# Performance work log

Measured on AMD Instinct MI355X. Metric: run time of the kernel, lower is better.

## Reference

```python
import jax, jax.numpy as jnp
import numpy as np

B, D_ENC, T = 4, 512, 200
D_DEC, U = 640, 100
H, V = 640, 1025


def setup_inputs() -> dict:
    key = jax.random.key(0)
    ks = jax.random.split(key, 8)
    s = lambda k, shape, fan: jax.random.normal(k, shape, dtype=jnp.float32) / np.sqrt(fan)
    return {
        "encoder_outputs": jax.random.normal(ks[0], (B, D_ENC, T), dtype=jnp.float32),
        "decoder_outputs": jax.random.normal(ks[1], (B, D_DEC, U), dtype=jnp.float32),
        "W_enc": s(ks[2], (D_ENC, H), D_ENC),
        "b_enc": jnp.zeros((H,), dtype=jnp.float32),
        "W_pred": s(ks[3], (D_DEC, H), D_DEC),
        "b_pred": jnp.zeros((H,), dtype=jnp.float32),
        "W_out": s(ks[4], (H, V), H),
        "b_out": jnp.zeros((V,), dtype=jnp.float32),
    }


def reference(encoder_outputs, decoder_outputs, W_enc, b_enc, W_pred, b_pred, W_out, b_out):
    # transpose(1,2): [B, D, T] -> [B, T, D], then linear projections to H
    enc_proj = jnp.einsum("bdt,dh->bth", encoder_outputs, W_enc) + b_enc   # [B, T, H]
    dec_proj = jnp.einsum("bdu,dh->buh", decoder_outputs, W_pred) + b_pred  # [B, U, H]
    # broadcast-sum: [B, T, 1, H] + [B, 1, U, H] -> [B, T, U, H]
    x = enc_proj[:, :, None, :] + dec_proj[:, None, :, :]
    x = jax.nn.relu(x)           # joint_net[0] activation; joint_net[1] dropout = identity (eval)
    out = jnp.einsum("btuh,hv->btuv", x, W_out) + b_out  # [B, T, U, V]
    return out
```

## Files before the change

kernel.cpp:

```cpp
#include <hip/hip_runtime.h>
#include <hip/hip_bf16.h>

#define B_   4
#define DENC 512
#define T_   200
#define DDEC 640
#define U_   100
#define H_   640
#define V_   1025
#define VPAD 1152

typedef float f32x4 __attribute__((ext_vector_type(4)));
typedef _Float16 f16x8 __attribute__((ext_vector_type(8)));
typedef unsigned short u16x8 __attribute__((ext_vector_type(8)));

__device__ __forceinline__ uint4 addrelu16(uint4 e, uint4 d) {
    f16x8 ev = __builtin_bit_cast(f16x8, e);
    f16x8 dv = __builtin_bit_cast(f16x8, d);
    f16x8 s = ev + dv;
    f16x8 z = {(_Float16)0.f, (_Float16)0.f, (_Float16)0.f, (_Float16)0.f,
               (_Float16)0.f, (_Float16)0.f, (_Float16)0.f, (_Float16)0.f};
    s = __builtin_elementwise_max(s, z);
    return __builtin_bit_cast(uint4, s);
}

__device__ __forceinline__ void gload_lds16(const void* g, void* l) {
    __builtin_amdgcn_global_load_lds(
        (const __attribute__((address_space(1))) unsigned int*)g,
        (__attribute__((address_space(3))) unsigned int*)l, 16, 0, 0);
}

__global__ __launch_bounds__(256) void prep_fused_kernel(
    const float* __restrict__ enc, const float* __restrict__ W_enc,
    const float* __restrict__ b_enc,
    const float* __restrict__ dec, const float* __restrict__ W_pred,
    const float* __restrict__ b_pred,
    const float* __restrict__ W_out,
    _Float16* __restrict__ encP, _Float16* __restrict__ decP,
    _Float16* __restrict__ Wt)
{
    __shared__ float tile[64][65];
    int bx = blockIdx.x;
    int tid = threadIdx.x;

    if (bx < 260) {
        int b = bx / 65, r5 = bx % 65, hc = r5 / 13, tg = r5 % 13;
        int h  = hc * 128 + (tid & 127);
        int t0 = tg * 16 + (tid >> 7) * 8;
        if (t0 >= T_) return;
        const float* ec = enc + (size_t)b * DENC * T_ + t0;
        const float* Wc = W_enc + h;
        float acc[8] = {0.f,0.f,0.f,0.f,0.f,0.f,0.f,0.f};
        #pragma unroll 8
        for (int d = 0; d < DENC; ++d) {
            float w = Wc[(size_t)d * H_];
            float4 e0 = *(const float4*)(ec + (size_t)d * T_);
            float4 e1 = *(const float4*)(ec + (size_t)d * T_ + 4);
            acc[0] += w * e0.x; acc[1] += w * e0.y; acc[2] += w * e0.z; acc[3] += w * e0.w;
            acc[4] += w * e1.x; acc[5] += w * e1.y; acc[6] += w * e1.z; acc[7] += w * e1.w;
        }
        float bb = b_enc[h];
        #pragma unroll
        for (int i = 0; i < 8; ++i)
            encP[((size_t)b * T_ + t0 + i) * H_ + h] = (_Float16)(acc[i] + bb);
    } else if (bx < 520) {
        int i5 = bx - 260;
        int b = i5 / 65, r5 = i5 % 65, hc = r5 / 13, ug = r5 % 13;
        int h  = hc * 128 + (tid & 127);
        int u0 = ug * 8 + (tid >> 7) * 4;
        if (u0 >= U_) return;
        const float* dc = dec + (size_t)b * DDEC * U_ + u0;
        const float* Wc = W_pred + h;
        float acc[4] = {0.f,0.f,0.f,0.f};
        #pragma unroll 8
        for (int d = 0; d < DDEC; ++d) {
            float w = Wc[(size_t)d * H_];
            float4 e0 = *(const float4*)(dc + (size_t)d * U_);
            acc[0] += w * e0.x; acc[1] += w * e0.y; acc[2] += w * e0.z; acc[3] += w * e0.w;
        }
        float bb = b_pred[h];
        #pragma unroll
        for (int i = 0; i < 4; ++i)
            decP[((size_t)b * U_ + u0 + i) * H_ + h] = (_Float16)(acc[i] + bb);
    } else {
        int j = bx - 520;
        int hc = j / 18, vc = j % 18;
        int h0 = hc * 64, v0 = vc * 64;
        #pragma unroll
        for (int it = 0; it < 16; ++it) {
            int hl = it * 4 + (tid >> 6);
            int vl = tid & 63;
            int v = v0 + vl;
            tile[hl][vl] = (v < V_) ? W_out[(size_t)(h0 + hl) * V_ + v] : 0.f;
        }
        __syncthreads();
        #pragma unroll
        for (int it = 0; it < 16; ++it) {
            int vl = it * 4 + (tid >> 6);
            int hl = tid & 63;
            Wt[(size_t)(v0 + vl) * H_ + h0 + hl] = (_Float16)tile[hl][vl];
        }
    }
}

#define ESTR 260
__global__ __launch_bounds__(256) void joint_kernel(
    const unsigned short* __restrict__ encP,
    const unsigned short* __restrict__ decP,
    const unsigned short* __restrict__ Wt,
    const float* __restrict__ b_out,
    float* __restrict__ out)
{
    __shared__ uint4 LA[2][64][4];
    __shared__ uint4 LB[2][256][4];
    int tid = threadIdx.x;

    if (blockIdx.x >= 5200) {
        int idx = (blockIdx.x - 5200) * 256 + tid;
        if (idx >= B_ * T_ * U_) return;
        int u = idx % U_;
        int t = (idx / U_) % T_;
        int b = idx / (U_ * T_);
        const uint4* e = (const uint4*)(encP + ((size_t)b * T_ + t) * H_);
        const uint4* d = (const uint4*)(decP + ((size_t)b * U_ + u) * H_);
        const uint4* wv = (const uint4*)(Wt + (size_t)1024 * H_);
        float acc1 = 0.f;
        for (int c = 0; c < H_ / 8; ++c) {
            f16x8 x = __builtin_bit_cast(f16x8, addrelu16(e[c], d[c]));
            f16x8 wq = __builtin_bit_cast(f16x8, wv[c]);
            #pragma unroll
            for (int m = 0; m < 8; ++m)
                acc1 += (float)x[m] * (float)wq[m];
        }
        out[((size_t)(b * T_ + t) * U_ + u) * V_ + 1024] = acc1 + b_out[1024];
        return;
    }

    int f   = blockIdx.x;
    int n   = (f & 7) * 650 + (f >> 3);
    int vi  = n / 1300;
    int rem = n - vi * 1300;
    int b   = rem / 325;
    int tu  = rem - b * 325;

    int tt = tu / 13, ut = tu % 13;
    int t0 = tt * 8, u0 = ut * 8, vb = vi * 256;
    int lane = tid & 63, w = tid >> 6;
    int lrow = lane & 15, kg = lane >> 4;

    int r  = tid >> 2, kc = tid & 3;
    int ta = t0 + (r >> 3);
    int ua = u0 + (r & 7); if (ua > U_ - 1) ua = U_ - 1;
    const unsigned short* eR = encP + ((size_t)b * T_ + ta) * H_ + kc * 8;
    const unsigned short* dR = decP + ((size_t)b * U_ + ua) * H_ + kc * 8;
    int fA = (r >> 1) & 3;

    int pcB = lane & 3;
    const unsigned short* gB[4];
    #pragma unroll
    for (int m = 0; m < 4; ++m) {
        int cl = w * 64 + m * 16 + (lane >> 2);
        gB[m] = Wt + (size_t)(vb + cl) * H_ + (pcB ^ ((cl >> 1) & 3)) * 8;
    }

    f32x4 acc[4][4];
    #pragma unroll
    for (int i = 0; i < 4; ++i)
        #pragma unroll
        for (int j = 0; j < 4; ++j)
            acc[i][j] = (f32x4){0.f, 0.f, 0.f, 0.f};

    {
        uint4 E = *(const uint4*)(eR);
        uint4 D = *(const uint4*)(dR);
        LA[0][r][kc ^ fA] = addrelu16(E, D);
        #pragma unroll
        for (int m = 0; m < 4; ++m)
            gload_lds16(gB[m], &LB[0][w * 64 + m * 16][0]);
    }
    __syncthreads();

    #pragma unroll 2
    for (int kt = 0; kt < 20; ++kt) {
        int cur = kt & 1;
        uint4 En, Dn;
        if (kt < 19) {
            En = *(const uint4*)(eR + (kt + 1) * 32);
            Dn = *(const uint4*)(dR + (kt + 1) * 32);
            #pragma unroll
            for (int m = 0; m < 4; ++m)
                gload_lds16(gB[m] + (kt + 1) * 32, &LB[cur ^ 1][w * 64 + m * 16][0]);
        }
        f16x8 a[4], bq[4];
        #pragma unroll
        for (int i = 0; i < 4; ++i) {
            int row = i * 16 + lrow;
            a[i] = __builtin_bit_cast(f16x8, LA[cur][row][kg ^ ((row >> 1) & 3)]);
        }
        #pragma unroll
        for (int j = 0; j < 4; ++j) {
            int col = w * 64 + j * 16 + lrow;
            bq[j] = __builtin_bit_cast(f16x8, LB[cur][col][kg ^ ((col >> 1) & 3)]);
        }
        #pragma unroll
        for (int i = 0; i < 4; ++i)
            #pragma unroll
            for (int j = 0; j < 4; ++j)
                acc[i][j] = __builtin_amdgcn_mfma_f32_16x16x32_f16(a[i], bq[j], acc[i][j], 0, 0, 0);
        if (kt < 19)
            LA[cur ^ 1][r][kc ^ fA] = addrelu16(En, Dn);
        __syncthreads();
    }

    float* etile = (float*)LB;
    #pragma unroll
    for (int i = 0; i < 4; ++i) {
        __syncthreads();
        #pragma unroll
        for (int j = 0; j < 4; ++j) {
            int col = w * 64 + j * 16 + lrow;
            float bo = b_out[vb + col];
            #pragma unroll
            for (int q = 0; q < 4; ++q)
                etile[(kg * 4 + q) * ESTR + col] = acc[i][j][q] + bo;
        }
        __syncthreads();
        #pragma unroll
        for (int rr = 0; rr < 4; ++rr) {
            int row16 = w * 4 + rr;
            int row = i * 16 + row16;
            int t = t0 + (row >> 3);
            int u = u0 + (row & 7);
            if (u < U_) {
                float* ob = &out[(((size_t)b * T_ + t) * U_ + u) * V_ + vb];
                const float* lb = &etile[row16 * ESTR];
                #pragma unroll
                for (int it = 0; it < 4; ++it)
                    ob[it * 64 + lane] = lb[it * 64 + lane];
            }
        }
    }
}

extern "C" void kernel_launch(void* const* d_in, const int* in_sizes, int n_in,
                              void* d_out, int out_size, void* d_ws, size_t ws_size,
                              hipStream_t stream) {
    const float* enc    = (const float*)d_in[0];
    const float* dec    = (const float*)d_in[1];
    const float* W_enc  = (const float*)d_in[2];
    const float* b_enc  = (const float*)d_in[3];
    const float* W_pred = (const float*)d_in[4];
    const float* b_pred = (const float*)d_in[5];
    const float* W_out  = (const float*)d_in[6];
    const float* b_out  = (const float*)d_in[7];
    float* out = (float*)d_out;

    char* ws = (char*)d_ws;
    _Float16* encP = (_Float16*)ws;
    _Float16* decP = (_Float16*)(ws + 1024000);
    _Float16* Wt   = (_Float16*)(ws + 1024000 + 512000);

    prep_fused_kernel<<<dim3(700), 256, 0, stream>>>(
        enc, W_enc, b_enc, dec, W_pred, b_pred, W_out, encP, decP, Wt);
    joint_kernel<<<dim3(5200 + (B_ * T_ * U_ + 255) / 256), 256, 0, stream>>>(
        (const unsigned short*)encP, (const unsigned short*)decP,
        (const unsigned short*)Wt, b_out, out);
}
```

Before: 271.8 us.

## Keep full-K W_out slice resident in LDS and stream A fragments from registers

The joint GEMM is restructured so each 512-thread block loads a 64-column slice of Wt across the whole H dimension into 80KB of dynamic LDS once, with an XOR swizzle. Each wave then builds its A fragments directly in registers from global enc/dec rows, applying the add+relu per k-step with two-deep register prefetch, so the per-iteration LDS A staging and the block barriers go away. The tile shape changes to 256 (t,u) rows by 64 V columns, which gives 5824 blocks. The trade-off is much higher LDS use per block, which may limit occupancy, narrower 64-float output stores, and repeated global reads of enc/dec rows across the V blocks.

```diff
diff --git a/kernel.cpp b/kernel.cpp
--- a/kernel.cpp
+++ b/kernel.cpp
@@ -8,11 +8,9 @@
 #define U_   100
 #define H_   640
 #define V_   1025
-#define VPAD 1152
 
 typedef float f32x4 __attribute__((ext_vector_type(4)));
 typedef _Float16 f16x8 __attribute__((ext_vector_type(8)));
-typedef unsigned short u16x8 __attribute__((ext_vector_type(8)));
 
 __device__ __forceinline__ uint4 addrelu16(uint4 e, uint4 d) {
     f16x8 ev = __builtin_bit_cast(f16x8, e);
@@ -103,20 +101,18 @@
     }
 }
 
-#define ESTR 260
-__global__ __launch_bounds__(256) void joint_kernel(
+__global__ __launch_bounds__(512, 4) void joint_kernel(
     const unsigned short* __restrict__ encP,
     const unsigned short* __restrict__ decP,
     const unsigned short* __restrict__ Wt,
     const float* __restrict__ b_out,
     float* __restrict__ out)
 {
-    __shared__ uint4 LA[2][64][4];
-    __shared__ uint4 LB[2][256][4];
+    extern __shared__ char LDSRAW[];
     int tid = threadIdx.x;
 
-    if (blockIdx.x >= 5200) {
-        int idx = (blockIdx.x - 5200) * 256 + tid;
+    if (blockIdx.x >= 5824) {
+        int idx = (blockIdx.x - 5824) * 512 + tid;
         if (idx >= B_ * T_ * U_) return;
         int u = idx % U_;
         int t = (idx / U_) % T_;
@@ -136,109 +132,99 @@
         return;
     }
 
-    int f   = blockIdx.x;
-    int n   = (f & 7) * 650 + (f >> 3);
-    int vi  = n / 1300;
-    int rem = n - vi * 1300;
-    int b   = rem / 325;
-    int tu  = rem - b * 325;
-
-    int tt = tu / 13, ut = tu % 13;
-    int t0 = tt * 8, u0 = ut * 8, vb = vi * 256;
+    int f    = blockIdx.x;
+    int n    = (f & 7) * 728 + (f >> 3);
+    int vblk = n / 364;
+    int rem  = n - vblk * 364;
+    int b    = rem / 91;
+    int y    = rem - b * 91;
+    int tt = y / 13, ut = y % 13;
+    int t0 = tt * 32, u0 = ut * 8;
+    int vb = vblk * 64;
     int lane = tid & 63, w = tid >> 6;
     int lrow = lane & 15, kg = lane >> 4;
 
-    int r  = tid >> 2, kc = tid & 3;
-    int ta = t0 + (r >> 3);
-    int ua = u0 + (r & 7); if (ua > U_ - 1) ua = U_ - 1;
-    const unsigned short* eR = encP + ((size_t)b * T_ + ta) * H_ + kc * 8;
-    const unsigned short* dR = decP + ((size_t)b * U_ + ua) * H_ + kc * 8;
-    int fA = (r >> 1) & 3;
-
-    int pcB = lane & 3;
-    const unsigned short* gB[4];
+    {
+        char* ldsb = LDSRAW + w * 10240;
+        #pragma unroll
+        for (int m = 0; m < 10; ++m) {
+            int flat = m * 64 + lane;
+            int cl = flat / 80, p = flat % 80;
+            int c  = p ^ (cl & 7);
+            const unsigned short* src = Wt + (size_t)(vb + w * 8 + cl) * H_ + c * 8;
+            gload_lds16(src, ldsb + m * 1024);
+        }
+    }
+    __syncthreads();
+
+    int row0 = w * 32 + lrow;
+    int tA0 = t0 + (row0 >> 3);        if (tA0 > T_ - 1) tA0 = T_ - 1;
+    int tA1 = t0 + ((row0 + 16) >> 3); if (tA1 > T_ - 1) tA1 = T_ - 1;
+    int uA  = u0 + (lrow & 7);         if (uA  > U_ - 1) uA  = U_ - 1;
+    const uint4* e0p = (const uint4*)(encP + ((size_t)b * T_ + tA0) * H_) + kg;
+    const uint4* e1p = (const uint4*)(encP + ((size_t)b * T_ + tA1) * H_) + kg;
+    const uint4* dp  = (const uint4*)(decP + ((size_t)b * U_ + uA ) * H_) + kg;
+
+    const char* LBb = LDSRAW;
+    int sB = (lrow & 7) << 4;
+    int bbase[4];
     #pragma unroll
-    for (int m = 0; m < 4; ++m) {
-        int cl = w * 64 + m * 16 + (lane >> 2);
-        gB[m] = Wt + (size_t)(vb + cl) * H_ + (pcB ^ ((cl >> 1) & 3)) * 8;
-    }
-
-    f32x4 acc[4][4];
+    for (int j = 0; j < 4; ++j) bbase[j] = (j * 16 + lrow) * 1280;
+
+    f32x4 acc[2][4];
     #pragma unroll
-    for (int i = 0; i < 4; ++i)
+    for (int i = 0; i < 2; ++i)
         #pragma unroll
         for (int j = 0; j < 4; ++j)
             acc[i][j] = (f32x4){0.f, 0.f, 0.f, 0.f};
 
-    {
-        uint4 E = *(const uint4*)(eR);
-        uint4 D = *(const uint4*)(dR);
-        LA[0][r][kc ^ fA] = addrelu16(E, D);
-        #pragma unroll
-        for (int m = 0; m < 4; ++m)
-            gload_lds16(gB[m], &LB[0][w * 64 + m * 16][0]);
-    }
+    uint4 E0a = e0p[0], E1a = e1p[0], Da = dp[0];
+    uint4 E0b = e0p[4], E1b = e1p[4], Db = dp[4];
+
+    #pragma unroll 2
+    for (int ks = 0; ks < 20; ++ks) {
+        f16x8 a0 = __builtin_bit_cast(f16x8, addrelu16(E0a, Da));
+        f16x8 a1 = __builtin_bit_cast(f16x8, addrelu16(E1a, Da));
+        E0a = E0b; E1a = E1b; Da = Db;
+        if (ks < 18) {
+            E0b = e0p[(ks + 2) * 4];
+            E1b = e1p[(ks + 2) * 4];
+            Db  = dp[(ks + 2) * 4];
+        }
+        int xoff = ((ks * 4 + kg) << 4) ^ sB;
+        f16x8 bq[4];
+        #pragma unroll
+        for (int j = 0; j < 4; ++j)
+            bq[j] = *(const f16x8*)(LBb + bbase[j] + xoff);
+        #pragma unroll
+        for (int j = 0; j < 4; ++j) {
+            acc[0][j] = __builtin_amdgcn_mfma_f32_16x16x32_f16(a0, bq[j], acc[0][j], 0, 0, 0);
+            acc[1][j] = __builtin_amdgcn_mfma_f32_16x16x32_f16(a1, bq[j], acc[1][j], 0, 0, 0);
+        }
+    }
+
     __syncthreads();
-
-    #pragma unroll 2
-    for (int kt = 0; kt < 20; ++kt) {
-        int cur = kt & 1;
-        uint4 En, Dn;
-        if (kt < 19) {
-            En = *(const uint4*)(eR + (kt + 1) * 32);
-            Dn = *(const uint4*)(dR + (kt + 1) * 32);
-            #pragma unroll
-            for (int m = 0; m < 4; ++m)
-                gload_lds16(gB[m] + (kt + 1) * 32, &LB[cur ^ 1][w * 64 + m * 16][0]);
-        }
-        f16x8 a[4], bq[4];
-        #pragma unroll
-        for (int i = 0; i < 4; ++i) {
-            int row = i * 16 + lrow;
-            a[i] = __builtin_bit_cast(f16x8, LA[cur][row][kg ^ ((row >> 1) & 3)]);
-        }
+    float* etile = (float*)LDSRAW + (size_t)w * 1088;
+    #pragma unroll
+    for (int i = 0; i < 2; ++i) {
         #pragma unroll
         for (int j = 0; j < 4; ++j) {
-            int col = w * 64 + j * 16 + lrow;
-            bq[j] = __builtin_bit_cast(f16x8, LB[cur][col][kg ^ ((col >> 1) & 3)]);
-        }
-        #pragma unroll
-        for (int i = 0; i < 4; ++i)
-            #pragma unroll
-            for (int j = 0; j < 4; ++j)
-                acc[i][j] = __builtin_amdgcn_mfma_f32_16x16x32_f16(a[i], bq[j], acc[i][j], 0, 0, 0);
-        if (kt < 19)
-            LA[cur ^ 1][r][kc ^ fA] = addrelu16(En, Dn);
-        __syncthreads();
-    }
-
-    float* etile = (float*)LB;
-    #pragma unroll
-    for (int i = 0; i < 4; ++i) {
-        __syncthreads();
-        #pragma unroll
-        for (int j = 0; j < 4; ++j) {
-            int col = w * 64 + j * 16 + lrow;
+            int col = j * 16 + lrow;
             float bo = b_out[vb + col];
             #pragma unroll
             for (int q = 0; q < 4; ++q)
-                etile[(kg * 4 + q) * ESTR + col] = acc[i][j][q] + bo;
+                etile[(kg * 4 + q) * 68 + col] = acc[i][j][q] + bo;
         }
         __syncthreads();
         #pragma unroll
-        for (int rr = 0; rr < 4; ++rr) {
-            int row16 = w * 4 + rr;
-            int row = i * 16 + row16;
+        for (int rr = 0; rr < 16; ++rr) {
+            int row = w * 32 + i * 16 + rr;
             int t = t0 + (row >> 3);
             int u = u0 + (row & 7);
-            if (u < U_) {
-                float* ob = &out[(((size_t)b * T_ + t) * U_ + u) * V_ + vb];
-                const float* lb = &etile[row16 * ESTR];
-                #pragma unroll
-                for (int it = 0; it < 4; ++it)
-                    ob[it * 64 + lane] = lb[it * 64 + lane];
-            }
-        }
+            if (t < T_ && u < U_)
+                out[(((size_t)b * T_ + t) * U_ + u) * V_ + vb + lane] = etile[rr * 68 + lane];
+        }
+        __syncthreads();
     }
 }
 
@@ -260,9 +246,12 @@
     _Float16* decP = (_Float16*)(ws + 1024000);
     _Float16* Wt   = (_Float16*)(ws + 1024000 + 512000);
 
+    (void)hipFuncSetAttribute((const void*)joint_kernel,
+                              hipFuncAttributeMaxDynamicSharedMemorySize, 81920);
+
     prep_fused_kernel<<<dim3(700), 256, 0, stream>>>(
         enc, W_enc, b_enc, dec, W_pred, b_pred, W_out, encP, decP, Wt);
-    joint_kernel<<<dim3(5200 + (B_ * T_ * U_ + 255) / 256), 256, 0, stream>>>(
+    joint_kernel<<<dim3(5824 + 157), 512, 81920, stream>>>(
         (const unsigned short*)encP, (const unsigned short*)decP,
         (const unsigned short*)Wt, b_out, out);
 }
```

After: 333.8 us. +22.8%, slower.

## Split projection reduction across warps with LDS reduce in prep kernel

Applied to the files above, without the earlier changes.

The encoder and decoder projection blocks now split the D reduction across the four wavefronts, with each thread accumulating more time/unit columns. Partial sums go into shared memory and are combined before the fp16 store. This raises the number of prep blocks and gives more memory-level parallelism in the small-GEMM prologue. The cost is an extra LDS round trip and a barrier.

```diff
diff --git a/kernel.cpp b/kernel.cpp
--- a/kernel.cpp
+++ b/kernel.cpp
@@ -12,7 +12,6 @@
 
 typedef float f32x4 __attribute__((ext_vector_type(4)));
 typedef _Float16 f16x8 __attribute__((ext_vector_type(8)));
-typedef unsigned short u16x8 __attribute__((ext_vector_type(8)));
 
 __device__ __forceinline__ uint4 addrelu16(uint4 e, uint4 d) {
     f16x8 ev = __builtin_bit_cast(f16x8, e);
@@ -39,53 +38,115 @@
     _Float16* __restrict__ encP, _Float16* __restrict__ decP,
     _Float16* __restrict__ Wt)
 {
-    __shared__ float tile[64][65];
+    __shared__ float sbuf[4224];
     int bx = blockIdx.x;
     int tid = threadIdx.x;
-
-    if (bx < 260) {
-        int b = bx / 65, r5 = bx % 65, hc = r5 / 13, tg = r5 % 13;
-        int h  = hc * 128 + (tid & 127);
-        int t0 = tg * 16 + (tid >> 7) * 8;
-        if (t0 >= T_) return;
+    int lane = tid & 63, w = tid >> 6;
+
+    if (bx < 520) {
+        int b = bx / 130, r5 = bx % 130, hc = r5 / 13, tg = r5 % 13;
+        int h  = hc * 64 + lane;
+        int t0 = tg * 16;
+        const float* Wc = W_enc + h;
         const float* ec = enc + (size_t)b * DENC * T_ + t0;
-        const float* Wc = W_enc + h;
-        float acc[8] = {0.f,0.f,0.f,0.f,0.f,0.f,0.f,0.f};
-        #pragma unroll 8
-        for (int d = 0; d < DENC; ++d) {
-            float w = Wc[(size_t)d * H_];
-            float4 e0 = *(const float4*)(ec + (size_t)d * T_);
-            float4 e1 = *(const float4*)(ec + (size_t)d * T_ + 4);
-            acc[0] += w * e0.x; acc[1] += w * e0.y; acc[2] += w * e0.z; acc[3] += w * e0.w;
-            acc[4] += w * e1.x; acc[5] += w * e1.y; acc[6] += w * e1.z; acc[7] += w * e1.w;
-        }
-        float bb = b_enc[h];
-        #pragma unroll
-        for (int i = 0; i < 8; ++i)
-            encP[((size_t)b * T_ + t0 + i) * H_ + h] = (_Float16)(acc[i] + bb);
-    } else if (bx < 520) {
-        int i5 = bx - 260;
-        int b = i5 / 65, r5 = i5 % 65, hc = r5 / 13, ug = r5 % 13;
-        int h  = hc * 128 + (tid & 127);
-        int u0 = ug * 8 + (tid >> 7) * 4;
-        if (u0 >= U_) return;
+        int d0 = w * 128;
+        float acc[16];
+        #pragma unroll
+        for (int i = 0; i < 16; ++i) acc[i] = 0.f;
+        if (t0 + 16 <= T_) {
+            #pragma unroll 8
+            for (int i = 0; i < 128; ++i) {
+                int d = d0 + i;
+                float wv = Wc[(size_t)d * H_];
+                const float* p = ec + (size_t)d * T_;
+                float4 a0 = *(const float4*)(p);
+                float4 a1 = *(const float4*)(p + 4);
+                float4 a2 = *(const float4*)(p + 8);
+                float4 a3 = *(const float4*)(p + 12);
+                acc[0]+=wv*a0.x; acc[1]+=wv*a0.y; acc[2]+=wv*a0.z; acc[3]+=wv*a0.w;
+                acc[4]+=wv*a1.x; acc[5]+=wv*a1.y; acc[6]+=wv*a1.z; acc[7]+=wv*a1.w;
+                acc[8]+=wv*a2.x; acc[9]+=wv*a2.y; acc[10]+=wv*a2.z; acc[11]+=wv*a2.w;
+                acc[12]+=wv*a3.x; acc[13]+=wv*a3.y; acc[14]+=wv*a3.z; acc[15]+=wv*a3.w;
+            }
+        } else {
+            #pragma unroll 8
+            for (int i = 0; i < 128; ++i) {
+                int d = d0 + i;
+                float wv = Wc[(size_t)d * H_];
+                const float* p = ec + (size_t)d * T_;
+                float4 a0 = *(const float4*)(p);
+                float4 a1 = *(const float4*)(p + 4);
+                acc[0]+=wv*a0.x; acc[1]+=wv*a0.y; acc[2]+=wv*a0.z; acc[3]+=wv*a0.w;
+                acc[4]+=wv*a1.x; acc[5]+=wv*a1.y; acc[6]+=wv*a1.z; acc[7]+=wv*a1.w;
+            }
+        }
+        #pragma unroll
+        for (int t = 0; t < 16; ++t)
+            sbuf[(w * 16 + t) * 66 + lane] = acc[t];
+        __syncthreads();
+        #pragma unroll
+        for (int k = 0; k < 4; ++k) {
+            int oi = tid + k * 256;
+            int t = oi >> 6, hl = oi & 63;
+            if (t0 + t < T_) {
+                float s = sbuf[(0 * 16 + t) * 66 + hl] + sbuf[(1 * 16 + t) * 66 + hl]
+                        + sbuf[(2 * 16 + t) * 66 + hl] + sbuf[(3 * 16 + t) * 66 + hl]
+                        + b_enc[hc * 64 + hl];
+                encP[((size_t)b * T_ + t0 + t) * H_ + hc * 64 + hl] = (_Float16)s;
+            }
+        }
+    } else if (bx < 1040) {
+        int i5 = bx - 520;
+        int b = i5 / 130, r5 = i5 % 130, hc = r5 / 13, ug = r5 % 13;
+        int h  = hc * 64 + lane;
+        int u0 = ug * 8;
+        const float* Wc = W_pred + h;
         const float* dc = dec + (size_t)b * DDEC * U_ + u0;
-        const float* Wc = W_pred + h;
-        float acc[4] = {0.f,0.f,0.f,0.f};
-        #pragma unroll 8
-        for (int d = 0; d < DDEC; ++d) {
-            float w = Wc[(size_t)d * H_];
-            float4 e0 = *(const float4*)(dc + (size_t)d * U_);
-            acc[0] += w * e0.x; acc[1] += w * e0.y; acc[2] += w * e0.z; acc[3] += w * e0.w;
-        }
-        float bb = b_pred[h];
-        #pragma unroll
-        for (int i = 0; i < 4; ++i)
-            decP[((size_t)b * U_ + u0 + i) * H_ + h] = (_Float16)(acc[i] + bb);
+        int d0 = w * 160;
+        float acc[8];
+        #pragma unroll
+        for (int i = 0; i < 8; ++i) acc[i] = 0.f;
+        if (u0 + 8 <= U_) {
+            #pragma unroll 8
+            for (int i = 0; i < 160; ++i) {
+                int d = d0 + i;
+                float wv = Wc[(size_t)d * H_];
+                const float* p = dc + (size_t)d * U_;
+                float4 a0 = *(const float4*)(p);
+                float4 a1 = *(const float4*)(p + 4);
+                acc[0]+=wv*a0.x; acc[1]+=wv*a0.y; acc[2]+=wv*a0.z; acc[3]+=wv*a0.w;
+                acc[4]+=wv*a1.x; acc[5]+=wv*a1.y; acc[6]+=wv*a1.z; acc[7]+=wv*a1.w;
+            }
+        } else {
+            #pragma unroll 8
+            for (int i = 0; i < 160; ++i) {
+                int d = d0 + i;
+                float wv = Wc[(size_t)d * H_];
+                const float* p = dc + (size_t)d * U_;
+                float4 a0 = *(const float4*)(p);
+                acc[0]+=wv*a0.x; acc[1]+=wv*a0.y; acc[2]+=wv*a0.z; acc[3]+=wv*a0.w;
+            }
+        }
+        #pragma unroll
+        for (int u = 0; u < 8; ++u)
+            sbuf[(w * 8 + u) * 66 + lane] = acc[u];
+        __syncthreads();
+        #pragma unroll
+        for (int k = 0; k < 2; ++k) {
+            int oi = tid + k * 256;
+            int u = oi >> 6, hl = oi & 63;
+            if (u0 + u < U_) {
+                float s = sbuf[(0 * 8 + u) * 66 + hl] + sbuf[(1 * 8 + u) * 66 + hl]
+                        + sbuf[(2 * 8 + u) * 66 + hl] + sbuf[(3 * 8 + u) * 66 + hl]
+                        + b_pred[hc * 64 + hl];
+                decP[((size_t)b * U_ + u0 + u) * H_ + hc * 64 + hl] = (_Float16)s;
+            }
+        }
     } else {
-        int j = bx - 520;
+        int j = bx - 1040;
         int hc = j / 18, vc = j % 18;
         int h0 = hc * 64, v0 = vc * 64;
+        float (*tile)[65] = (float(*)[65])sbuf;
         #pragma unroll
         for (int it = 0; it < 16; ++it) {
             int hl = it * 4 + (tid >> 6);
@@ -260,7 +321,7 @@
     _Float16* decP = (_Float16*)(ws + 1024000);
     _Float16* Wt   = (_Float16*)(ws + 1024000 + 512000);
 
-    prep_fused_kernel<<<dim3(700), 256, 0, stream>>>(
+    prep_fused_kernel<<<dim3(1220), 256, 0, stream>>>(
         enc, W_enc, b_enc, dec, W_pred, b_pred, W_out, encP, decP, Wt);
     joint_kernel<<<dim3(5200 + (B_ * T_ * U_ + 255) / 256), 256, 0, stream>>>(
         (const unsigned short*)encP, (const unsigned short*)decP,
```

Result: faster. 251.9 us (-7.3%).
